# Kernel optimization log

Hardware: AMD Instinct MI355X
Metric: run time of the kernel (lower is better)

## Reference

```python
import jax, jax.numpy as jnp
import numpy as np


def setup_inputs() -> dict:
    key = jax.random.key(0)
    ks = jax.random.split(key, 7)
    B = 32768
    x = jax.random.normal(ks[0], (B, 1, 28, 28), dtype=jnp.float32)
    # learned params (AtomicLinear weight/bias per layer)
    w1 = jax.random.normal(ks[1], (128, 784), dtype=jnp.float32)
    b1 = jax.random.normal(ks[2], (128,), dtype=jnp.float32)
    w2 = jax.random.normal(ks[3], (256, 128), dtype=jnp.float32)
    b2 = jax.random.normal(ks[4], (256,), dtype=jnp.float32)
    w3 = jax.random.normal(ks[5], (10, 256), dtype=jnp.float32)
    b3 = jax.random.normal(ks[6], (10,), dtype=jnp.float32)
    return {"x": x, "w1": w1, "b1": b1, "w2": w2, "b2": b2, "w3": w3, "b3": b3}


def reference(x, w1, b1, w2, b2, w3, b3):
    # AtomicLinear: (x[:,None,:] * W) gathered by a random permutation over
    # in_features, then summed over that axis. Summation is permutation-
    # invariant, so this is exactly x @ W.T + b.
    B = x.shape[0]
    h = x.reshape(B, -1)                      # [B, 784]
    h = jax.nn.relu(h @ w1.T + b1)            # [B, 128]
    h = jax.nn.relu(h @ w2.T + b2)            # [B, 256]
    logits = h @ w3.T + b3                    # [B, 10]
    return jax.nn.log_softmax(logits, axis=1)
```

## Files before the change

kernel.cpp:

```cpp
#include <hip/hip_runtime.h>
#include <hip/hip_bf16.h>
#include <math.h>


#define TPB 1024

typedef __attribute__((ext_vector_type(8))) short bf16x8;
typedef __attribute__((ext_vector_type(4))) float f32x4;

static __device__ inline short f2bf(float f) {
    union { float f; unsigned u; } v; v.f = f;
    unsigned r = v.u + 0x7fffu + ((v.u >> 16) & 1u);
    return (short)(r >> 16);
}
static __device__ inline bf16x8 cvt8(float4 a, float4 b) {
    union { __hip_bfloat162 h2[4]; bf16x8 v; } u;
    u.h2[0] = __float22bfloat162_rn(make_float2(a.x, a.y));
    u.h2[1] = __float22bfloat162_rn(make_float2(a.z, a.w));
    u.h2[2] = __float22bfloat162_rn(make_float2(b.x, b.y));
    u.h2[3] = __float22bfloat162_rn(make_float2(b.z, b.w));
    return u.v;
}
static __device__ inline float4 ld4g(const float* p, bool ok) {
    return ok ? *reinterpret_cast<const float4*>(p) : make_float4(0.f,0.f,0.f,0.f);
}

__global__ __launch_bounds__(TPB, 4) void mnist_v6(
    const float* __restrict__ x,
    const float* __restrict__ w1,
    const float* __restrict__ b1v,
    const float* __restrict__ w2,
    const float* __restrict__ b2v,
    const float* __restrict__ w3,
    const float* __restrict__ b3v,
    float* __restrict__ out)
{
    __shared__ __align__(16) char smem[72 * 1024];
    short* const s_wt = (short*)smem;
    short* const s_h1 = (short*)(smem + 32 * 1024);
    short* const s_w3 = (short*)(smem + 64 * 1024);
    short* const s_h2 = (short*)smem;

    const int t    = threadIdx.x;
    const int lane = t & 63;
    const int wv   = t >> 6;
    const int mi   = wv >> 1;
    const int nh   = wv & 1;
    const int l15  = lane & 15;
    const int l4   = lane >> 4;
    const int r0   = blockIdx.x * 128;

    const int sn = t >> 3, ss = t & 7;
    const int un = t >> 2, us = t & 3;

    const float* xrow = &x[(size_t)(r0 + mi * 16 + l15) * 784];

    {
        const float* p = &w1[(size_t)sn * 784 + ss * 8];
        const float4 a = ld4g(p, true), b = ld4g(p + 4, true);
        *(bf16x8*)&s_wt[sn * 64 + ((ss ^ (sn & 7)) << 3)] = cvt8(a, b);
    }
    float4 xc0 = ld4g(xrow + l4 * 8, true);
    float4 xc1 = ld4g(xrow + l4 * 8 + 4, true);
    float4 xc2 = ld4g(xrow + 32 + l4 * 8, true);
    float4 xc3 = ld4g(xrow + 32 + l4 * 8 + 4, true);
    __syncthreads();

    f32x4 acc1[4];
    #pragma unroll
    for (int nf = 0; nf < 4; ++nf) acc1[nf] = (f32x4){0.f,0.f,0.f,0.f};

    for (int kt = 0; kt < 13; ++kt) {
        short* const rbuf = s_wt + (kt & 1) * 8192;
        short* const nbuf = s_wt + ((kt & 1) ^ 1) * 8192;
        float4 xn0, xn1, xn2, xn3, wf0, wf1;
        if (kt < 12) {
            const int kb = (kt + 1) * 64;
            const int k1 = kb + l4 * 8, k2 = kb + 32 + l4 * 8;
            xn0 = ld4g(xrow + k1, k1 + 8 <= 784);
            xn1 = ld4g(xrow + k1 + 4, k1 + 8 <= 784);
            xn2 = ld4g(xrow + k2, k2 + 8 <= 784);
            xn3 = ld4g(xrow + k2 + 4, k2 + 8 <= 784);
            const int kw = kb + ss * 8;
            const float* p = &w1[(size_t)sn * 784 + kw];
            const bool ok = kw + 8 <= 784;
            wf0 = ld4g(p, ok);
            wf1 = ld4g(p + 4, ok);
        }
        const bf16x8 a0 = cvt8(xc0, xc1);
        const bf16x8 a1 = cvt8(xc2, xc3);
        #pragma unroll
        for (int nf = 0; nf < 4; ++nf) {
            const int rB = nh * 64 + nf * 16 + l15;
            const bf16x8 b0 = *(const bf16x8*)&rbuf[rB * 64 + (((0 + l4) ^ (rB & 7)) << 3)];
            const bf16x8 b1 = *(const bf16x8*)&rbuf[rB * 64 + (((4 + l4) ^ (rB & 7)) << 3)];
            acc1[nf] = __builtin_amdgcn_mfma_f32_16x16x32_bf16(a0, b0, acc1[nf], 0, 0, 0);
            acc1[nf] = __builtin_amdgcn_mfma_f32_16x16x32_bf16(a1, b1, acc1[nf], 0, 0, 0);
        }
        if (kt < 12) {
            *(bf16x8*)&nbuf[sn * 64 + ((ss ^ (sn & 7)) << 3)] = cvt8(wf0, wf1);
            xc0 = xn0; xc1 = xn1; xc2 = xn2; xc3 = xn3;
        }
        __syncthreads();
    }

    #pragma unroll
    for (int nf = 0; nf < 4; ++nf) {
        const int c = nh * 64 + nf * 16 + l15;
        const float bc = b1v[c];
        #pragma unroll
        for (int i = 0; i < 4; ++i) {
            const int r = mi * 16 + l4 * 4 + i;
            const float h = fmaxf(acc1[nf][i] + bc, 0.f);
            s_h1[r * 128 + (((c >> 3) ^ (r & 7)) << 3) + (c & 7)] = f2bf(h);
        }
    }
    {
        const float* p = &w2[(size_t)un * 128 + us * 8];
        const float4 wa = ld4g(p, true), wb = ld4g(p + 4, true);
        float4 w3a = make_float4(0,0,0,0), w3b = w3a;
        const int n3 = t >> 5, s3 = t & 31;
        if (t < 512 && n3 < 10) {
            const float* q = &w3[(size_t)n3 * 256 + s3 * 8];
            w3a = ld4g(q, true); w3b = ld4g(q + 4, true);
        }
        *(bf16x8*)&s_wt[8192 + un * 32 + ((us ^ (un & 3)) << 3)] = cvt8(wa, wb);
        if (t < 512)
            *(bf16x8*)&s_w3[n3 * 256 + ((s3 ^ (n3 & 7)) << 3)] = cvt8(w3a, w3b);
    }
    __syncthreads();

    bf16x8 a2[4];
    {
        const int row = mi * 16 + l15;
        #pragma unroll
        for (int kk = 0; kk < 4; ++kk)
            a2[kk] = *(const bf16x8*)&s_h1[row * 128 + (((kk * 4 + l4) ^ (row & 7)) << 3)];
    }
    f32x4 acc2[8];
    #pragma unroll
    for (int nf = 0; nf < 8; ++nf) acc2[nf] = (f32x4){0.f,0.f,0.f,0.f};

    #pragma unroll
    for (int kt = 0; kt < 4; ++kt) {
        short* const rbuf = s_wt + (((kt + 1) & 1)) * 8192;
        short* const wbuf = s_wt + ((kt & 1)) * 8192;
        float4 wa, wb;
        if (kt < 3) {
            const float* p = &w2[(size_t)un * 128 + (kt + 1) * 32 + us * 8];
            wa = ld4g(p, true); wb = ld4g(p + 4, true);
        }
        #pragma unroll
        for (int nf = 0; nf < 8; ++nf) {
            const int rB = nh * 128 + nf * 16 + l15;
            const bf16x8 b = *(const bf16x8*)&rbuf[rB * 32 + ((l4 ^ (rB & 3)) << 3)];
            acc2[nf] = __builtin_amdgcn_mfma_f32_16x16x32_bf16(a2[kt], b, acc2[nf], 0, 0, 0);
        }
        if (kt < 3)
            *(bf16x8*)&wbuf[un * 32 + ((us ^ (un & 3)) << 3)] = cvt8(wa, wb);
        __syncthreads();
    }

    #pragma unroll
    for (int nf = 0; nf < 8; ++nf) {
        const int c = nh * 128 + nf * 16 + l15;
        const float bc = b2v[c];
        #pragma unroll
        for (int i = 0; i < 4; ++i) {
            const int r = mi * 16 + l4 * 4 + i;
            const float h = fmaxf(acc2[nf][i] + bc, 0.f);
            s_h2[r * 256 + (((c >> 3) ^ (r & 7)) << 3) + (c & 7)] = f2bf(h);
        }
    }
    __syncthreads();

    if (nh == 0) {
        const int row = mi * 16 + l15;
        f32x4 acc3 = (f32x4){0.f,0.f,0.f,0.f};
        #pragma unroll
        for (int kt = 0; kt < 8; ++kt) {
            const int slot = kt * 4 + l4;
            const bf16x8 a3 = *(const bf16x8*)&s_h2[row * 256 + ((slot ^ (row & 7)) << 3)];
            const bf16x8 b3r = *(const bf16x8*)&s_w3[l15 * 256 + ((slot ^ (l15 & 7)) << 3)];
            acc3 = __builtin_amdgcn_mfma_f32_16x16x32_bf16(a3, b3r, acc3, 0, 0, 0);
        }
        const float b3c = (l15 < 10) ? b3v[l15] : 0.f;
        #pragma unroll
        for (int i = 0; i < 4; ++i) {
            const float v = acc3[i] + b3c;
            float m = (l15 < 10) ? v : -1e30f;
            #pragma unroll
            for (int off = 8; off; off >>= 1) m = fmaxf(m, __shfl_xor(m, off, 16));
            const float e = (l15 < 10) ? expf(v - m) : 0.f;
            float sum = e;
            #pragma unroll
            for (int off = 8; off; off >>= 1) sum += __shfl_xor(sum, off, 16);
            const float ls = m + logf(sum);
            if (l15 < 10) {
                const int r = r0 + mi * 16 + l4 * 4 + i;
                out[(size_t)r * 10 + l15] = v - ls;
            }
        }
    }
}

extern "C" void kernel_launch(void* const* d_in, const int* in_sizes, int n_in,
                              void* d_out, int out_size, void* d_ws, size_t ws_size,
                              hipStream_t stream) {
    const float* x  = (const float*)d_in[0];
    const float* w1 = (const float*)d_in[1];
    const float* b1 = (const float*)d_in[2];
    const float* w2 = (const float*)d_in[3];
    const float* b2 = (const float*)d_in[4];
    const float* w3 = (const float*)d_in[5];
    const float* b3 = (const float*)d_in[6];
    float* out = (float*)d_out;

    dim3 grid(32768 / 128), block(TPB);
    mnist_v6<<<grid, block, 0, stream>>>(x, w1, b1, w2, b2, w3, b3, out);
}
```

Baseline: 38.11 us.

## Prepack weights to swizzled bf16 and stream tiles via global_load_lds

Adds a small prep kernel that converts w1/w2/w3 to bf16 in the exact swizzled tile layout into workspace each call. The main kernel then stages x (fp32) and weight tiles directly into LDS with async global_load_lds, double-buffered, instead of register loads, converts and LDS stores. Block size halves to 512 threads with 64 rows per block, doubling the grid. This is meant to cut per-block fp32-to-bf16 weight conversion and register staging, at the cost of an extra kernel launch and more LDS per block.

```diff
diff --git a/kernel.cpp b/kernel.cpp
--- a/kernel.cpp
+++ b/kernel.cpp
@@ -3,7 +3,11 @@
 #include <math.h>
 
 
-#define TPB 1024
+#define TPB 512
+
+#define W2K 106496
+#define W3K 139264
+#define NCHUNK_TOT 17920
 
 typedef __attribute__((ext_vector_type(8))) short bf16x8;
 typedef __attribute__((ext_vector_type(4))) float f32x4;
@@ -24,22 +28,63 @@
 static __device__ inline float4 ld4g(const float* p, bool ok) {
     return ok ? *reinterpret_cast<const float4*>(p) : make_float4(0.f,0.f,0.f,0.f);
 }
-
-__global__ __launch_bounds__(TPB, 4) void mnist_v6(
+static __device__ inline void gld16(const void* g, void* l) {
+    __builtin_amdgcn_global_load_lds(
+        (const __attribute__((address_space(1))) unsigned int*)g,
+        (__attribute__((address_space(3))) unsigned int*)l, 16, 0, 0);
+}
+
+__global__ void prep_pack(const float* __restrict__ w1,
+                          const float* __restrict__ w2,
+                          const float* __restrict__ w3,
+                          short* __restrict__ wb) {
+    const int tid = blockIdx.x * blockDim.x + threadIdx.x;
+    if (tid >= NCHUNK_TOT) return;
+    float4 a = make_float4(0,0,0,0), b = a;
+    size_t dst;
+    if (tid < 13312) {
+        const int kt = tid >> 10, rem = tid & 1023, row = rem >> 3, phys = rem & 7;
+        const int kg = kt * 64 + ((phys ^ (row & 7)) << 3);
+        if (kg + 8 <= 784) {
+            const float* p = &w1[(size_t)row * 784 + kg];
+            a = *(const float4*)p; b = *(const float4*)(p + 4);
+        }
+        dst = (size_t)tid * 8;
+    } else if (tid < 17408) {
+        const int t2 = tid - 13312;
+        const int kt = t2 >> 10, rem = t2 & 1023, row = rem >> 2, phys = rem & 3;
+        const int kg = kt * 32 + ((phys ^ (row & 3)) << 3);
+        const float* p = &w2[(size_t)row * 128 + kg];
+        a = *(const float4*)p; b = *(const float4*)(p + 4);
+        dst = (size_t)W2K + (size_t)t2 * 8;
+    } else {
+        const int t3 = tid - 17408;
+        const int row = t3 >> 5, phys = t3 & 31;
+        const int kg = (phys ^ (row & 7)) << 3;
+        if (row < 10) {
+            const float* p = &w3[(size_t)row * 256 + kg];
+            a = *(const float4*)p; b = *(const float4*)(p + 4);
+        }
+        dst = (size_t)W3K + (size_t)t3 * 8;
+    }
+    *(bf16x8*)&wb[dst] = cvt8(a, b);
+}
+
+__global__ __launch_bounds__(TPB, 4) void mnist_v8(
     const float* __restrict__ x,
-    const float* __restrict__ w1,
     const float* __restrict__ b1v,
-    const float* __restrict__ w2,
     const float* __restrict__ b2v,
-    const float* __restrict__ w3,
     const float* __restrict__ b3v,
+    const short* __restrict__ wb,
     float* __restrict__ out)
 {
-    __shared__ __align__(16) char smem[72 * 1024];
-    short* const s_wt = (short*)smem;
-    short* const s_h1 = (short*)(smem + 32 * 1024);
-    short* const s_w3 = (short*)(smem + 64 * 1024);
-    short* const s_h2 = (short*)smem;
+    __shared__ __align__(16) char smem[80 * 1024];
+    float* const xb  = (float*)smem;
+    short* const wbf = (short*)(smem + 32 * 1024);
+    short* const h1  = (short*)(smem + 64 * 1024);
+    short* const w2l = (short*)smem;
+    short* const h2  = wbf;
+    short* const w3l = h1;
 
     const int t    = threadIdx.x;
     const int lane = t & 63;
@@ -48,22 +93,37 @@
     const int nh   = wv & 1;
     const int l15  = lane & 15;
     const int l4   = lane >> 4;
-    const int r0   = blockIdx.x * 128;
-
-    const int sn = t >> 3, ss = t & 7;
-    const int un = t >> 2, us = t & 3;
-
-    const float* xrow = &x[(size_t)(r0 + mi * 16 + l15) * 784];
-
-    {
-        const float* p = &w1[(size_t)sn * 784 + ss * 8];
-        const float4 a = ld4g(p, true), b = ld4g(p + 4, true);
-        *(bf16x8*)&s_wt[sn * 64 + ((ss ^ (sn & 7)) << 3)] = cvt8(a, b);
-    }
-    float4 xc0 = ld4g(xrow + l4 * 8, true);
-    float4 xc1 = ld4g(xrow + l4 * 8 + 4, true);
-    float4 xc2 = ld4g(xrow + 32 + l4 * 8, true);
-    float4 xc3 = ld4g(xrow + 32 + l4 * 8 + 4, true);
+    const int row0 = blockIdx.x * 64;
+
+    const size_t XLAST = (size_t)32768 * 3136 - 16;
+
+    auto stage_x = [&](int kt, float* dst) {
+        #pragma unroll
+        for (int p = 0; p < 2; ++p) {
+            const int rloc = wv * 8 + p * 4;
+            size_t off = (size_t)(row0 + rloc + (lane >> 4)) * 3136
+                       + (size_t)kt * 256 + (size_t)(lane & 15) * 16;
+            if (off > XLAST) off = XLAST;
+            gld16((const char*)x + off, dst + rloc * 64);
+        }
+    };
+    auto stage_w1 = [&](int kt, short* dst) {
+        #pragma unroll
+        for (int p = 0; p < 2; ++p) {
+            const int rloc = wv * 16 + p * 8;
+            gld16(wb + (size_t)kt * 8192 + rloc * 64 + lane * 8, dst + rloc * 64);
+        }
+    };
+    auto stage_w2 = [&](int kt, short* dst) {
+        #pragma unroll
+        for (int p = 0; p < 2; ++p) {
+            const int rloc = wv * 32 + p * 16;
+            gld16(wb + W2K + (size_t)kt * 8192 + rloc * 32 + lane * 8, dst + rloc * 32);
+        }
+    };
+
+    stage_x(0, xb);
+    stage_w1(0, wbf);
     __syncthreads();
 
     f32x4 acc1[4];
@@ -71,39 +131,30 @@
     for (int nf = 0; nf < 4; ++nf) acc1[nf] = (f32x4){0.f,0.f,0.f,0.f};
 
     for (int kt = 0; kt < 13; ++kt) {
-        short* const rbuf = s_wt + (kt & 1) * 8192;
-        short* const nbuf = s_wt + ((kt & 1) ^ 1) * 8192;
-        float4 xn0, xn1, xn2, xn3, wf0, wf1;
+        const int cur = kt & 1;
         if (kt < 12) {
-            const int kb = (kt + 1) * 64;
-            const int k1 = kb + l4 * 8, k2 = kb + 32 + l4 * 8;
-            xn0 = ld4g(xrow + k1, k1 + 8 <= 784);
-            xn1 = ld4g(xrow + k1 + 4, k1 + 8 <= 784);
-            xn2 = ld4g(xrow + k2, k2 + 8 <= 784);
-            xn3 = ld4g(xrow + k2 + 4, k2 + 8 <= 784);
-            const int kw = kb + ss * 8;
-            const float* p = &w1[(size_t)sn * 784 + kw];
-            const bool ok = kw + 8 <= 784;
-            wf0 = ld4g(p, ok);
-            wf1 = ld4g(p + 4, ok);
-        }
-        const bf16x8 a0 = cvt8(xc0, xc1);
-        const bf16x8 a1 = cvt8(xc2, xc3);
-        #pragma unroll
-        for (int nf = 0; nf < 4; ++nf) {
-            const int rB = nh * 64 + nf * 16 + l15;
-            const bf16x8 b0 = *(const bf16x8*)&rbuf[rB * 64 + (((0 + l4) ^ (rB & 7)) << 3)];
-            const bf16x8 b1 = *(const bf16x8*)&rbuf[rB * 64 + (((4 + l4) ^ (rB & 7)) << 3)];
-            acc1[nf] = __builtin_amdgcn_mfma_f32_16x16x32_bf16(a0, b0, acc1[nf], 0, 0, 0);
-            acc1[nf] = __builtin_amdgcn_mfma_f32_16x16x32_bf16(a1, b1, acc1[nf], 0, 0, 0);
-        }
-        if (kt < 12) {
-            *(bf16x8*)&nbuf[sn * 64 + ((ss ^ (sn & 7)) << 3)] = cvt8(wf0, wf1);
-            xc0 = xn0; xc1 = xn1; xc2 = xn2; xc3 = xn3;
+            stage_x(kt + 1, xb + (cur ^ 1) * 4096);
+            stage_w1(kt + 1, wbf + (cur ^ 1) * 8192);
+        }
+        const float* xt = xb + cur * 4096;
+        const short* wt = wbf + cur * 8192;
+        #pragma unroll
+        for (int kk = 0; kk < 2; ++kk) {
+            const float* ap = &xt[(16 * mi + l15) * 64 + kk * 32 + l4 * 8];
+            const bf16x8 a = cvt8(*(const float4*)ap, *(const float4*)(ap + 4));
+            #pragma unroll
+            for (int nf = 0; nf < 4; ++nf) {
+                const int rB = nh * 64 + nf * 16 + l15;
+                const int phys = (kk * 4 + l4) ^ (rB & 7);
+                const bf16x8 b = *(const bf16x8*)&wt[rB * 64 + phys * 8];
+                acc1[nf] = __builtin_amdgcn_mfma_f32_16x16x32_bf16(a, b, acc1[nf], 0, 0, 0);
+            }
         }
         __syncthreads();
     }
 
+    stage_w2(0, w2l);
+    stage_w2(1, w2l + 8192);
     #pragma unroll
     for (int nf = 0; nf < 4; ++nf) {
         const int c = nh * 64 + nf * 16 + l15;
@@ -112,21 +163,8 @@
         for (int i = 0; i < 4; ++i) {
             const int r = mi * 16 + l4 * 4 + i;
             const float h = fmaxf(acc1[nf][i] + bc, 0.f);
-            s_h1[r * 128 + (((c >> 3) ^ (r & 7)) << 3) + (c & 7)] = f2bf(h);
-        }
-    }
-    {
-        const float* p = &w2[(size_t)un * 128 + us * 8];
-        const float4 wa = ld4g(p, true), wb = ld4g(p + 4, true);
-        float4 w3a = make_float4(0,0,0,0), w3b = w3a;
-        const int n3 = t >> 5, s3 = t & 31;
-        if (t < 512 && n3 < 10) {
-            const float* q = &w3[(size_t)n3 * 256 + s3 * 8];
-            w3a = ld4g(q, true); w3b = ld4g(q + 4, true);
-        }
-        *(bf16x8*)&s_wt[8192 + un * 32 + ((us ^ (un & 3)) << 3)] = cvt8(wa, wb);
-        if (t < 512)
-            *(bf16x8*)&s_w3[n3 * 256 + ((s3 ^ (n3 & 7)) << 3)] = cvt8(w3a, w3b);
+            h1[r * 128 + (((c >> 3) ^ (r & 7)) << 3) + (c & 7)] = f2bf(h);
+        }
     }
     __syncthreads();
 
@@ -135,30 +173,32 @@
         const int row = mi * 16 + l15;
         #pragma unroll
         for (int kk = 0; kk < 4; ++kk)
-            a2[kk] = *(const bf16x8*)&s_h1[row * 128 + (((kk * 4 + l4) ^ (row & 7)) << 3)];
-    }
+            a2[kk] = *(const bf16x8*)&h1[row * 128 + (((kk * 4 + l4) ^ (row & 7)) << 3)];
+    }
+    __syncthreads();
+
+    {
+        const int rloc = wv * 2;
+        gld16(wb + W3K + rloc * 256 + lane * 8, w3l + rloc * 256);
+    }
+
     f32x4 acc2[8];
     #pragma unroll
     for (int nf = 0; nf < 8; ++nf) acc2[nf] = (f32x4){0.f,0.f,0.f,0.f};
 
     #pragma unroll
     for (int kt = 0; kt < 4; ++kt) {
-        short* const rbuf = s_wt + (((kt + 1) & 1)) * 8192;
-        short* const wbuf = s_wt + ((kt & 1)) * 8192;
-        float4 wa, wb;
-        if (kt < 3) {
-            const float* p = &w2[(size_t)un * 128 + (kt + 1) * 32 + us * 8];
-            wa = ld4g(p, true); wb = ld4g(p + 4, true);
-        }
+        const short* wt2 = w2l + (kt & 1) * 8192;
         #pragma unroll
         for (int nf = 0; nf < 8; ++nf) {
             const int rB = nh * 128 + nf * 16 + l15;
-            const bf16x8 b = *(const bf16x8*)&rbuf[rB * 32 + ((l4 ^ (rB & 3)) << 3)];
+            const int phys = l4 ^ (rB & 3);
+            const bf16x8 b = *(const bf16x8*)&wt2[rB * 32 + phys * 8];
             acc2[nf] = __builtin_amdgcn_mfma_f32_16x16x32_bf16(a2[kt], b, acc2[nf], 0, 0, 0);
         }
-        if (kt < 3)
-            *(bf16x8*)&wbuf[un * 32 + ((us ^ (un & 3)) << 3)] = cvt8(wa, wb);
         __syncthreads();
+        if (kt < 2)
+            stage_w2(kt + 2, w2l + (kt & 1) * 8192);
     }
 
     #pragma unroll
@@ -169,7 +209,7 @@
         for (int i = 0; i < 4; ++i) {
             const int r = mi * 16 + l4 * 4 + i;
             const float h = fmaxf(acc2[nf][i] + bc, 0.f);
-            s_h2[r * 256 + (((c >> 3) ^ (r & 7)) << 3) + (c & 7)] = f2bf(h);
+            h2[r * 256 + (((c >> 3) ^ (r & 7)) << 3) + (c & 7)] = f2bf(h);
         }
     }
     __syncthreads();
@@ -180,8 +220,8 @@
         #pragma unroll
         for (int kt = 0; kt < 8; ++kt) {
             const int slot = kt * 4 + l4;
-            const bf16x8 a3 = *(const bf16x8*)&s_h2[row * 256 + ((slot ^ (row & 7)) << 3)];
-            const bf16x8 b3r = *(const bf16x8*)&s_w3[l15 * 256 + ((slot ^ (l15 & 7)) << 3)];
+            const bf16x8 a3  = *(const bf16x8*)&h2[row * 256 + ((slot ^ (row & 7)) << 3)];
+            const bf16x8 b3r = *(const bf16x8*)&w3l[l15 * 256 + ((slot ^ (l15 & 7)) << 3)];
             acc3 = __builtin_amdgcn_mfma_f32_16x16x32_bf16(a3, b3r, acc3, 0, 0, 0);
         }
         const float b3c = (l15 < 10) ? b3v[l15] : 0.f;
@@ -197,7 +237,7 @@
             for (int off = 8; off; off >>= 1) sum += __shfl_xor(sum, off, 16);
             const float ls = m + logf(sum);
             if (l15 < 10) {
-                const int r = r0 + mi * 16 + l4 * 4 + i;
+                const int r = row0 + mi * 16 + l4 * 4 + i;
                 out[(size_t)r * 10 + l15] = v - ls;
             }
         }
@@ -215,7 +255,10 @@
     const float* w3 = (const float*)d_in[5];
     const float* b3 = (const float*)d_in[6];
     float* out = (float*)d_out;
-
-    dim3 grid(32768 / 128), block(TPB);
-    mnist_v6<<<grid, block, 0, stream>>>(x, w1, b1, w2, b2, w3, b3, out);
-}
+    short* wb  = (short*)d_ws;
+
+    prep_pack<<<(NCHUNK_TOT + 255) / 256, 256, 0, stream>>>(w1, w2, w3, wb);
+
+    dim3 grid(32768 / 64), block(TPB);
+    mnist_v8<<<grid, block, 0, stream>>>(x, b1, b2, b3, wb, out);
+}
```

Measured after the change: 62.68 us. +64.5%, slower.
